# Kernel tuning notes

Measured on AMD Instinct MI355X. Metric: run time of the kernel, lower is better.

The kernel has to match this reference:

```python
import jax, jax.numpy as jnp
import numpy as np

N = 262144  # collocation points
H = 128     # hidden width


def setup_inputs() -> dict:
    key = jax.random.key(0)
    ks = jax.random.split(key, 9)
    def glorot(k, shape):
        fan_in = shape[0]
        return jax.random.normal(k, shape, dtype=jnp.float32) / jnp.sqrt(jnp.float32(fan_in))
    return {
        "x": jax.random.normal(ks[0], (N, 3), dtype=jnp.float32),
        "W1": glorot(ks[1], (3, H)), "b1": jnp.zeros((H,), jnp.float32),
        "W2": glorot(ks[2], (H, H)), "b2": jnp.zeros((H,), jnp.float32),
        "W3": glorot(ks[3], (H, H)), "b3": jnp.zeros((H,), jnp.float32),
        "W4": glorot(ks[4], (H, 1)), "b4": jnp.zeros((1,), jnp.float32),
    }


def reference(x, W1, b1, W2, b2, W3, b3, W4, b4):
    def f(xi):  # xi: (3,) -> scalar c
        h = jnp.tanh(xi @ W1 + b1)
        h = jnp.tanh(h @ W2 + b2)
        h = jnp.tanh(h @ W3 + b3)
        return (h @ W4 + b4)[0]

    # forward value and full first-order gradient per point
    c, g = jax.vmap(jax.value_and_grad(f))(x)  # c: (N,), g: (N, 3)
    dc_dt, dc_dx, dc_dy = g[:, 0], g[:, 1], g[:, 2]

    # diagonal Hessian entries via forward-over-reverse HVPs
    e_x = jnp.array([0.0, 1.0, 0.0], dtype=x.dtype)
    e_y = jnp.array([0.0, 0.0, 1.0], dtype=x.dtype)

    def hvp(xi, v):
        return jax.jvp(jax.grad(f), (xi,), (v,))[1]

    d2c_dx2 = jax.vmap(lambda xi: hvp(xi, e_x)[1])(x)  # (N,)
    d2c_dy2 = jax.vmap(lambda xi: hvp(xi, e_y)[2])(x)  # (N,)

    return (c[:, None], dc_dt, dc_dx, dc_dy, d2c_dx2, d2c_dy2)
```

## Files before the change

### kernel.cpp

```cpp
#include <hip/hip_runtime.h>
#include <hip/hip_bf16.h>

#define TPB  256
#define WPB  4
#define NBLK 256
#define PROW 136
#define PSZ  (128 * PROW)

typedef short    short8 __attribute__((ext_vector_type(8)));
typedef float    f32x4  __attribute__((ext_vector_type(4)));
typedef unsigned uint4v __attribute__((ext_vector_type(4)));

#define SBAR() __builtin_amdgcn_sched_barrier(0)

struct Frag   { short8 k0, k1, k2, k3; };
struct Acc8   { f32x4 n0, n1, n2, n3, n4, n5, n6, n7; };
struct Acc8x6 { Acc8 a, b, c, d, e, f; };

__device__ __forceinline__ f32x4 sp4(float v) { f32x4 r = {v, v, v, v}; return r; }

__device__ __forceinline__ float fast_tanh(float z) {
    float e = __expf(2.0f * z);
    return 1.0f - 2.0f * __builtin_amdgcn_rcpf(e + 1.0f);
}
__device__ __forceinline__ f32x4 tanh4(f32x4 z) {
    f32x4 r;
    r[0] = fast_tanh(z[0]); r[1] = fast_tanh(z[1]);
    r[2] = fast_tanh(z[2]); r[3] = fast_tanh(z[3]);
    return r;
}

__device__ __forceinline__ unsigned short bf16_bits(float v) {
    __hip_bfloat16 b = __float2bfloat16(v);
    unsigned short s; __builtin_memcpy(&s, &b, 2);
    return s;
}
__device__ __forceinline__ unsigned pack_bf2(float lo, float hi) {
    unsigned r;
    asm("v_cvt_pk_bf16_f32 %0, %1, %2" : "=v"(r) : "v"(lo), "v"(hi));
    return r;
}
__device__ __forceinline__ short8 packB(f32x4 lo, f32x4 hi) {
    uint4v u;
    u[0] = pack_bf2(lo[0], lo[1]);
    u[1] = pack_bf2(lo[2], lo[3]);
    u[2] = pack_bf2(hi[0], hi[1]);
    u[3] = pack_bf2(hi[2], hi[3]);
    return __builtin_bit_cast(short8, u);
}

__device__ __forceinline__ Acc8 acc_zero() {
    Acc8 A;
    A.n0 = sp4(0.f); A.n1 = sp4(0.f); A.n2 = sp4(0.f); A.n3 = sp4(0.f);
    A.n4 = sp4(0.f); A.n5 = sp4(0.f); A.n6 = sp4(0.f); A.n7 = sp4(0.f);
    return A;
}
__device__ __forceinline__ Acc8 acc_bias(const float* bp, int fb) {
    Acc8 A;
    A.n0 = *(const f32x4*)(bp + 0 * 16 + fb);
    A.n1 = *(const f32x4*)(bp + 1 * 16 + fb);
    A.n2 = *(const f32x4*)(bp + 2 * 16 + fb);
    A.n3 = *(const f32x4*)(bp + 3 * 16 + fb);
    A.n4 = *(const f32x4*)(bp + 4 * 16 + fb);
    A.n5 = *(const f32x4*)(bp + 5 * 16 + fb);
    A.n6 = *(const f32x4*)(bp + 6 * 16 + fb);
    A.n7 = *(const f32x4*)(bp + 7 * 16 + fb);
    return A;
}

__device__ __forceinline__ Acc8x6 gemm6_frag(const unsigned short* __restrict__ pnl,
                                             int c, int g,
                                             Frag B0, Frag B1, Frag B2,
                                             Frag B3, Frag B4, Frag B5,
                                             Acc8 A0, Acc8 A1, Acc8 A2,
                                             Acc8 A3, Acc8 A4, Acc8 A5) {
#define ROW6(NT, N, KK, V0, V1, V2, V3, V4, V5) { \
    const short8 af = *reinterpret_cast<const short8*>( \
        pnl + ((NT) * 16 + c) * PROW + (KK) * 32 + g * 8); \
    A0.N = __builtin_amdgcn_mfma_f32_16x16x32_bf16(af, V0, A0.N, 0, 0, 0); \
    A1.N = __builtin_amdgcn_mfma_f32_16x16x32_bf16(af, V1, A1.N, 0, 0, 0); \
    A2.N = __builtin_amdgcn_mfma_f32_16x16x32_bf16(af, V2, A2.N, 0, 0, 0); \
    A3.N = __builtin_amdgcn_mfma_f32_16x16x32_bf16(af, V3, A3.N, 0, 0, 0); \
    A4.N = __builtin_amdgcn_mfma_f32_16x16x32_bf16(af, V4, A4.N, 0, 0, 0); \
    A5.N = __builtin_amdgcn_mfma_f32_16x16x32_bf16(af, V5, A5.N, 0, 0, 0); }
#define KS6(KK, V0, V1, V2, V3, V4, V5) \
    ROW6(0, n0, KK, V0, V1, V2, V3, V4, V5) ROW6(1, n1, KK, V0, V1, V2, V3, V4, V5) \
    ROW6(2, n2, KK, V0, V1, V2, V3, V4, V5) ROW6(3, n3, KK, V0, V1, V2, V3, V4, V5) \
    ROW6(4, n4, KK, V0, V1, V2, V3, V4, V5) ROW6(5, n5, KK, V0, V1, V2, V3, V4, V5) \
    ROW6(6, n6, KK, V0, V1, V2, V3, V4, V5) ROW6(7, n7, KK, V0, V1, V2, V3, V4, V5)
    KS6(0, B0.k0, B1.k0, B2.k0, B3.k0, B4.k0, B5.k0)
    KS6(1, B0.k1, B1.k1, B2.k1, B3.k1, B4.k1, B5.k1)
    SBAR();
    KS6(2, B0.k2, B1.k2, B2.k2, B3.k2, B4.k2, B5.k2)
    KS6(3, B0.k3, B1.k3, B2.k3, B3.k3, B4.k3, B5.k3)
    SBAR();
#undef KS6
#undef ROW6
    Acc8x6 R; R.a = A0; R.b = A1; R.c = A2; R.d = A3; R.e = A4; R.f = A5; return R;
}

__device__ __forceinline__ float red16(float v) {
    v += __shfl_xor(v, 16, 64);
    v += __shfl_xor(v, 32, 64);
    return v;
}
__device__ __forceinline__ float hsum4(f32x4 v) {
    return (v[0] + v[1]) + (v[2] + v[3]);
}

__global__ __launch_bounds__(TPB, 1) __attribute__((amdgpu_waves_per_eu(1)))
void mlp_jet_kernel(
    const float* __restrict__ X,
    const float* __restrict__ gW1, const float* __restrict__ gB1,
    const float* __restrict__ gW2, const float* __restrict__ gB2,
    const float* __restrict__ gW3, const float* __restrict__ gB3,
    const float* __restrict__ gW4, const float* __restrict__ gB4,
    float* __restrict__ out, int N)
{
    __shared__ alignas(16) unsigned short sPanel[2 * PSZ];
    __shared__ alignas(16) float sParam[7 * 128];

    const int tid = threadIdx.x;
    for (int idx = tid; idx < 2 * 128 * 128; idx += TPB) {
        int p = idx >> 14, e = idx & 16383, n = e >> 7, pp = e & 127;
        int kk = pp >> 5, gg = (pp >> 3) & 3, jj = pp & 7;
        int f = ((((jj >> 2) << 2) | kk) << 4) | (gg << 2) | (jj & 3);
        const float* Wsrc = p ? gW3 : gW2;
        sPanel[p * PSZ + n * PROW + pp] = bf16_bits(Wsrc[f * 128 + n]);
    }
    if (tid < 128) {
        sParam[0 * 128 + tid] = gW1[tid];
        sParam[1 * 128 + tid] = gW1[128 + tid];
        sParam[2 * 128 + tid] = gW1[256 + tid];
        sParam[3 * 128 + tid] = gB1[tid];
        sParam[4 * 128 + tid] = gB2[tid];
        sParam[5 * 128 + tid] = gB3[tid];
        sParam[6 * 128 + tid] = gW4[tid];
    }
    __syncthreads();

    const int lane = tid & 63;
    const int wave = tid >> 6;
    const int c = lane & 15, g = lane >> 4;
    const int fb = g << 2;
    const unsigned short* const pW2f = sPanel;
    const unsigned short* const pW3f = sPanel + PSZ;
    const float b4 = gB4[0];
    const float* const w4p = sParam + 6 * 128;

    const int tiles = N >> 4;
    for (int t = blockIdx.x * WPB + wave; t < tiles; t += NBLK * WPB) {
        const int sbase = t << 4;
        const float* xp = X + (long)(sbase + c) * 3;
        const float xt = xp[0], xx = xp[1], xy = xp[2];

        Frag h1F, t1t, t1x, t1y, s1x, s1y;
#define SEED(K, IL, IH) { \
    const int fL = (IL) * 16 + fb, fH = (IH) * 16 + fb; \
    f32x4 wtL = *(const f32x4*)(sParam + fL),        wtH = *(const f32x4*)(sParam + fH); \
    f32x4 wxL = *(const f32x4*)(sParam + 128 + fL),  wxH = *(const f32x4*)(sParam + 128 + fH); \
    f32x4 wyL = *(const f32x4*)(sParam + 256 + fL),  wyH = *(const f32x4*)(sParam + 256 + fH); \
    f32x4 bbL = *(const f32x4*)(sParam + 384 + fL),  bbH = *(const f32x4*)(sParam + 384 + fH); \
    f32x4 hL = tanh4(sp4(xt) * wtL + sp4(xx) * wxL + sp4(xy) * wyL + bbL); \
    f32x4 hH = tanh4(sp4(xt) * wtH + sp4(xx) * wxH + sp4(xy) * wyH + bbH); \
    f32x4 aL = sp4(1.f) - hL * hL, aH = sp4(1.f) - hH * hH; \
    h1F.K = packB(hL, hH); \
    t1t.K = packB(aL * wtL, aH * wtH); \
    t1x.K = packB(aL * wxL, aH * wxH); \
    t1y.K = packB(aL * wyL, aH * wyH); \
    s1x.K = packB((sp4(0.f) - hL) * aL * wxL * wxL, (sp4(0.f) - hH) * aH * wxH * wxH); \
    s1y.K = packB((sp4(0.f) - hL) * aL * wyL * wyL, (sp4(0.f) - hH) * aH * wyH * wyH); }
        SEED(k0, 0, 4) SEED(k1, 1, 5) SEED(k2, 2, 6) SEED(k3, 3, 7)
#undef SEED

        Acc8x6 R6 = gemm6_frag(pW2f, c, g, h1F, t1t, t1x, t1y, s1x, s1y,
                               acc_bias(sParam + 4 * 128, fb),
                               acc_zero(), acc_zero(), acc_zero(),
                               acc_zero(), acc_zero());

        Frag h2F, t2t, txF, tyF, s2xF, s2yF;
#define POST2(K, NL, NH) { \
    f32x4 hL = tanh4(R6.a.NL), hH = tanh4(R6.a.NH); \
    f32x4 aL = sp4(1.f) - hL * hL, aH = sp4(1.f) - hH * hH; \
    h2F.K = packB(hL, hH); \
    t2t.K = packB(aL * R6.b.NL, aH * R6.b.NH); \
    f32x4 txL = aL * R6.c.NL, txH = aH * R6.c.NH; \
    txF.K = packB(txL, txH); \
    f32x4 pxL = (sp4(0.f) - hL) * txL * R6.c.NL, pxH = (sp4(0.f) - hH) * txH * R6.c.NH; \
    f32x4 tyL = aL * R6.d.NL, tyH = aH * R6.d.NH; \
    tyF.K = packB(tyL, tyH); \
    f32x4 pyL = (sp4(0.f) - hL) * tyL * R6.d.NL, pyH = (sp4(0.f) - hH) * tyH * R6.d.NH; \
    s2xF.K = packB(aL * R6.e.NL + pxL, aH * R6.e.NH + pxH); \
    s2yF.K = packB(aL * R6.f.NL + pyL, aH * R6.f.NH + pyH); }
        POST2(k0, n0, n4) POST2(k1, n1, n5) POST2(k2, n2, n6) POST2(k3, n3, n7)
#undef POST2

        R6 = gemm6_frag(pW3f, c, g, h2F, t2t, txF, tyF, s2xF, s2yF,
                        acc_bias(sParam + 5 * 128, fb),
                        acc_zero(), acc_zero(), acc_zero(),
                        acc_zero(), acc_zero());

        {
            f32x4 scp = sp4(0.f), sc1t = sp4(0.f);
            f32x4 srxa = sp4(0.f), srxb = sp4(0.f);
            f32x4 srya = sp4(0.f), sryb = sp4(0.f);
            f32x4 sc2x = sp4(0.f), sc2y = sp4(0.f);
#define DOTS(NL, NH, IL, IH) { \
    f32x4 w4L = *(const f32x4*)(w4p + (IL) * 16 + fb); \
    f32x4 w4H = *(const f32x4*)(w4p + (IH) * 16 + fb); \
    f32x4 hL = tanh4(R6.a.NL), hH = tanh4(R6.a.NH); \
    f32x4 waL = w4L * (sp4(1.f) - hL * hL), waH = w4H * (sp4(1.f) - hH * hH); \
    scp  += w4L * hL + w4H * hH; \
    sc1t += waL * R6.b.NL + waH * R6.b.NH; \
    f32x4 wtxL = waL * R6.c.NL, wtxH = waH * R6.c.NH; \
    srxa += wtxL + wtxH; \
    srxb -= wtxL * hL * R6.c.NL + wtxH * hH * R6.c.NH; \
    f32x4 wtyL = waL * R6.d.NL, wtyH = waH * R6.d.NH; \
    srya += wtyL + wtyH; \
    sryb -= wtyL * hL * R6.d.NL + wtyH * hH * R6.d.NH; \
    sc2x += waL * R6.e.NL + waH * R6.e.NH; \
    sc2y += waL * R6.f.NL + waH * R6.f.NH; }
            DOTS(n0, n4, 0, 4) DOTS(n1, n5, 1, 5) DOTS(n2, n6, 2, 6) DOTS(n3, n7, 3, 7)
#undef DOTS
            float cp  = red16(hsum4(scp));
            float c1t = red16(hsum4(sc1t));
            float c1x = red16(hsum4(srxa));
            float c1y = red16(hsum4(srya));
            float c2x = red16(hsum4(srxb) + hsum4(sc2x));
            float c2y = red16(hsum4(sryb) + hsum4(sc2y));
            if (lane < 16) {
                out[sbase + lane]           = cp + b4;
                out[(long)N + sbase + lane] = c1t;
                out[2L * N + sbase + lane]  = c1x;
                out[3L * N + sbase + lane]  = c1y;
                out[4L * N + sbase + lane]  = 2.f * c2x;
                out[5L * N + sbase + lane]  = 2.f * c2y;
            }
        }
    }
}

extern "C" void kernel_launch(void* const* d_in, const int* in_sizes, int n_in,
                              void* d_out, int out_size, void* d_ws, size_t ws_size,
                              hipStream_t stream) {
    const float* X  = (const float*)d_in[0];
    const float* W1 = (const float*)d_in[1];
    const float* B1 = (const float*)d_in[2];
    const float* W2 = (const float*)d_in[3];
    const float* B2 = (const float*)d_in[4];
    const float* W3 = (const float*)d_in[5];
    const float* B3 = (const float*)d_in[6];
    const float* W4 = (const float*)d_in[7];
    const float* B4 = (const float*)d_in[8];
    float* out = (float*)d_out;
    const int N = in_sizes[0] / 3;

    mlp_jet_kernel<<<NBLK, TPB, 0, stream>>>(X, W1, B1, W2, B2, W3, B3, W4, B4, out, N);
}
```

Measured before the change: 134.0 us.

## Interleave per-tile MFMA phases with tanh epilogue to overlap matrix and vector work

Instead of running the full 6-way GEMM for a layer and then the whole tanh/derivative epilogue, the GEMM is split into four phases, each covering two output tiles across all K. After each phase, the elementwise post-processing (POST2 or DOTS) for those tiles runs. This lets VALU transcendental work overlap with MFMA work from the next phase and may cut live accumulator pressure, but the sched_barriers limit how far the compiler can reorder, and the A-fragment loads are now issued per phase.

```diff
diff --git a/kernel.cpp b/kernel.cpp
--- a/kernel.cpp
+++ b/kernel.cpp
@@ -47,6 +47,9 @@
     u[2] = pack_bf2(hi[0], hi[1]);
     u[3] = pack_bf2(hi[2], hi[3]);
     return __builtin_bit_cast(short8, u);
+}
+__device__ __forceinline__ f32x4 mfma(short8 a, short8 b, f32x4 c) {
+    return __builtin_amdgcn_mfma_f32_16x16x32_bf16(a, b, c, 0, 0, 0);
 }
 
 __device__ __forceinline__ Acc8 acc_zero() {
@@ -66,37 +69,6 @@
     A.n6 = *(const f32x4*)(bp + 6 * 16 + fb);
     A.n7 = *(const f32x4*)(bp + 7 * 16 + fb);
     return A;
-}
-
-__device__ __forceinline__ Acc8x6 gemm6_frag(const unsigned short* __restrict__ pnl,
-                                             int c, int g,
-                                             Frag B0, Frag B1, Frag B2,
-                                             Frag B3, Frag B4, Frag B5,
-                                             Acc8 A0, Acc8 A1, Acc8 A2,
-                                             Acc8 A3, Acc8 A4, Acc8 A5) {
-#define ROW6(NT, N, KK, V0, V1, V2, V3, V4, V5) { \
-    const short8 af = *reinterpret_cast<const short8*>( \
-        pnl + ((NT) * 16 + c) * PROW + (KK) * 32 + g * 8); \
-    A0.N = __builtin_amdgcn_mfma_f32_16x16x32_bf16(af, V0, A0.N, 0, 0, 0); \
-    A1.N = __builtin_amdgcn_mfma_f32_16x16x32_bf16(af, V1, A1.N, 0, 0, 0); \
-    A2.N = __builtin_amdgcn_mfma_f32_16x16x32_bf16(af, V2, A2.N, 0, 0, 0); \
-    A3.N = __builtin_amdgcn_mfma_f32_16x16x32_bf16(af, V3, A3.N, 0, 0, 0); \
-    A4.N = __builtin_amdgcn_mfma_f32_16x16x32_bf16(af, V4, A4.N, 0, 0, 0); \
-    A5.N = __builtin_amdgcn_mfma_f32_16x16x32_bf16(af, V5, A5.N, 0, 0, 0); }
-#define KS6(KK, V0, V1, V2, V3, V4, V5) \
-    ROW6(0, n0, KK, V0, V1, V2, V3, V4, V5) ROW6(1, n1, KK, V0, V1, V2, V3, V4, V5) \
-    ROW6(2, n2, KK, V0, V1, V2, V3, V4, V5) ROW6(3, n3, KK, V0, V1, V2, V3, V4, V5) \
-    ROW6(4, n4, KK, V0, V1, V2, V3, V4, V5) ROW6(5, n5, KK, V0, V1, V2, V3, V4, V5) \
-    ROW6(6, n6, KK, V0, V1, V2, V3, V4, V5) ROW6(7, n7, KK, V0, V1, V2, V3, V4, V5)
-    KS6(0, B0.k0, B1.k0, B2.k0, B3.k0, B4.k0, B5.k0)
-    KS6(1, B0.k1, B1.k1, B2.k1, B3.k1, B4.k1, B5.k1)
-    SBAR();
-    KS6(2, B0.k2, B1.k2, B2.k2, B3.k2, B4.k2, B5.k2)
-    KS6(3, B0.k3, B1.k3, B2.k3, B3.k3, B4.k3, B5.k3)
-    SBAR();
-#undef KS6
-#undef ROW6
-    Acc8x6 R; R.a = A0; R.b = A1; R.c = A2; R.d = A3; R.e = A4; R.f = A5; return R;
 }
 
 __device__ __forceinline__ float red16(float v) {
@@ -173,10 +145,24 @@
         SEED(k0, 0, 4) SEED(k1, 1, 5) SEED(k2, 2, 6) SEED(k3, 3, 7)
 #undef SEED
 
-        Acc8x6 R6 = gemm6_frag(pW2f, c, g, h1F, t1t, t1x, t1y, s1x, s1y,
-                               acc_bias(sParam + 4 * 128, fb),
-                               acc_zero(), acc_zero(), acc_zero(),
-                               acc_zero(), acc_zero());
+        Acc8x6 R6;
+        R6.a = acc_bias(sParam + 4 * 128, fb);
+        R6.b = acc_zero(); R6.c = acc_zero(); R6.d = acc_zero();
+        R6.e = acc_zero(); R6.f = acc_zero();
+#define MROW(PNL, NT, N, KK, F0, F1, F2, F3, F4, F5) { \
+    const short8 af = *reinterpret_cast<const short8*>( \
+        PNL + ((NT) * 16 + c) * PROW + (KK) * 32 + g * 8); \
+    R6.a.N = mfma(af, F0.k##KK, R6.a.N); \
+    R6.b.N = mfma(af, F1.k##KK, R6.b.N); \
+    R6.c.N = mfma(af, F2.k##KK, R6.c.N); \
+    R6.d.N = mfma(af, F3.k##KK, R6.d.N); \
+    R6.e.N = mfma(af, F4.k##KK, R6.e.N); \
+    R6.f.N = mfma(af, F5.k##KK, R6.f.N); }
+#define MPHASE(PNL, NTa, Na, NTb, Nb, F0, F1, F2, F3, F4, F5) \
+    MROW(PNL, NTa, Na, 0, F0,F1,F2,F3,F4,F5) MROW(PNL, NTa, Na, 1, F0,F1,F2,F3,F4,F5) \
+    MROW(PNL, NTa, Na, 2, F0,F1,F2,F3,F4,F5) MROW(PNL, NTa, Na, 3, F0,F1,F2,F3,F4,F5) \
+    MROW(PNL, NTb, Nb, 0, F0,F1,F2,F3,F4,F5) MROW(PNL, NTb, Nb, 1, F0,F1,F2,F3,F4,F5) \
+    MROW(PNL, NTb, Nb, 2, F0,F1,F2,F3,F4,F5) MROW(PNL, NTb, Nb, 3, F0,F1,F2,F3,F4,F5)
 
         Frag h2F, t2t, txF, tyF, s2xF, s2yF;
 #define POST2(K, NL, NH) { \
@@ -192,19 +178,29 @@
     f32x4 pyL = (sp4(0.f) - hL) * tyL * R6.d.NL, pyH = (sp4(0.f) - hH) * tyH * R6.d.NH; \
     s2xF.K = packB(aL * R6.e.NL + pxL, aH * R6.e.NH + pxH); \
     s2yF.K = packB(aL * R6.f.NL + pyL, aH * R6.f.NH + pyH); }
-        POST2(k0, n0, n4) POST2(k1, n1, n5) POST2(k2, n2, n6) POST2(k3, n3, n7)
+
+        MPHASE(pW2f, 0, n0, 4, n4, h1F, t1t, t1x, t1y, s1x, s1y)
+        SBAR();
+        POST2(k0, n0, n4)
+        MPHASE(pW2f, 1, n1, 5, n5, h1F, t1t, t1x, t1y, s1x, s1y)
+        SBAR();
+        POST2(k1, n1, n5)
+        MPHASE(pW2f, 2, n2, 6, n6, h1F, t1t, t1x, t1y, s1x, s1y)
+        SBAR();
+        POST2(k2, n2, n6)
+        MPHASE(pW2f, 3, n3, 7, n7, h1F, t1t, t1x, t1y, s1x, s1y)
+        SBAR();
+        POST2(k3, n3, n7)
 #undef POST2
 
-        R6 = gemm6_frag(pW3f, c, g, h2F, t2t, txF, tyF, s2xF, s2yF,
-                        acc_bias(sParam + 5 * 128, fb),
-                        acc_zero(), acc_zero(), acc_zero(),
-                        acc_zero(), acc_zero());
-
-        {
-            f32x4 scp = sp4(0.f), sc1t = sp4(0.f);
-            f32x4 srxa = sp4(0.f), srxb = sp4(0.f);
-            f32x4 srya = sp4(0.f), sryb = sp4(0.f);
-            f32x4 sc2x = sp4(0.f), sc2y = sp4(0.f);
+        R6.a = acc_bias(sParam + 5 * 128, fb);
+        R6.b = acc_zero(); R6.c = acc_zero(); R6.d = acc_zero();
+        R6.e = acc_zero(); R6.f = acc_zero();
+
+        f32x4 scp = sp4(0.f), sc1t = sp4(0.f);
+        f32x4 srxa = sp4(0.f), srxb = sp4(0.f);
+        f32x4 srya = sp4(0.f), sryb = sp4(0.f);
+        f32x4 sc2x = sp4(0.f), sc2y = sp4(0.f);
 #define DOTS(NL, NH, IL, IH) { \
     f32x4 w4L = *(const f32x4*)(w4p + (IL) * 16 + fb); \
     f32x4 w4H = *(const f32x4*)(w4p + (IH) * 16 + fb); \
@@ -220,8 +216,24 @@
     sryb -= wtyL * hL * R6.d.NL + wtyH * hH * R6.d.NH; \
     sc2x += waL * R6.e.NL + waH * R6.e.NH; \
     sc2y += waL * R6.f.NL + waH * R6.f.NH; }
-            DOTS(n0, n4, 0, 4) DOTS(n1, n5, 1, 5) DOTS(n2, n6, 2, 6) DOTS(n3, n7, 3, 7)
+
+        MPHASE(pW3f, 0, n0, 4, n4, h2F, t2t, txF, tyF, s2xF, s2yF)
+        SBAR();
+        DOTS(n0, n4, 0, 4)
+        MPHASE(pW3f, 1, n1, 5, n5, h2F, t2t, txF, tyF, s2xF, s2yF)
+        SBAR();
+        DOTS(n1, n5, 1, 5)
+        MPHASE(pW3f, 2, n2, 6, n6, h2F, t2t, txF, tyF, s2xF, s2yF)
+        SBAR();
+        DOTS(n2, n6, 2, 6)
+        MPHASE(pW3f, 3, n3, 7, n7, h2F, t2t, txF, tyF, s2xF, s2yF)
+        SBAR();
+        DOTS(n3, n7, 3, 7)
 #undef DOTS
+#undef MPHASE
+#undef MROW
+
+        {
             float cp  = red16(hsum4(scp));
             float c1t = red16(hsum4(sc1t));
             float c1x = red16(hsum4(srxa));
```

New measurement: 139.7 us. 4.2% more time.
